# Kernel optimization log

Measured on AMD Instinct MI355X. Metric: run time of the kernel, lower is better.

## Reference

```python
import jax, jax.numpy as jnp
import numpy as np

D = 2048   # hidden_d
V = 2048   # hidden_v
L = 512    # number of points in seq
P = 64     # len(positions); decode steps = P + 1 (final special-symbol step)


def setup_inputs() -> dict:
    key = jax.random.key(0)
    ks = jax.random.split(key, 10)
    s = 0.02  # init scale for weights
    return dict(
        initial_state=jax.random.normal(ks[0], (1, D), dtype=jnp.float32),
        encoder_states=jax.random.normal(ks[1], (L + 1, D), dtype=jnp.float32),
        seq_points=jax.random.normal(ks[2], (L, 3), dtype=jnp.float32),
        positions=jax.random.randint(ks[3], (P,), 0, L),
        # LSTMCell params (torch layout: gates ordered i,f,g,o)
        W_ih=jax.random.normal(ks[4], (4 * D, 3), dtype=jnp.float32) * s,
        W_hh=jax.random.normal(ks[5], (4 * D, D), dtype=jnp.float32) * s,
        b_ih=jnp.zeros((4 * D,), dtype=jnp.float32),
        b_hh=jnp.zeros((4 * D,), dtype=jnp.float32),
        # Pointer params
        We_w=jax.random.normal(ks[6], (V, D), dtype=jnp.float32) * s,
        We_b=jnp.zeros((V,), dtype=jnp.float32),
        Wd_w=jax.random.normal(ks[7], (V, D), dtype=jnp.float32) * s,
        Wd_b=jnp.zeros((V,), dtype=jnp.float32),
        v_w=jax.random.normal(ks[8], (1, V), dtype=jnp.float32) * s,
        v_b=jnp.zeros((1,), dtype=jnp.float32),
    )


def reference(initial_state, encoder_states, seq_points, positions,
              W_ih, W_hh, b_ih, b_hh, We_w, We_b, Wd_w, Wd_b, v_w, v_b):
    """Teacher-forced pointer-network decode (positions given).

    Returns (logits [T, L+1], hidden_states [T, D], losses [T]) with
    T = len(positions) + 1 (final step targets the special symbol).
    """
    special = jnp.array([0.0, 0.0, 1.0], dtype=seq_points.dtype)
    stack_seq = jnp.concatenate([seq_points, special[None]], axis=0)  # [L+1, 3]
    Lseq = seq_points.shape[0]

    # teacher-forced inputs: step 0 = special symbol, step t = seq[positions[t-1]]
    xs = jnp.concatenate([special[None], stack_seq[positions]], axis=0)  # [T, 3]
    targets = jnp.concatenate([positions, jnp.array([Lseq])], axis=0)    # [T]

    # encoder projection is step-invariant: hoist out of the loop
    enc_proj = encoder_states @ We_w.T + We_b  # [L+1, V]

    h0 = initial_state[0]            # [D]
    c0 = jnp.zeros_like(h0)

    def step(carry, inp):
        h, c = carry
        x, tgt = inp
        gates = W_ih @ x + b_ih + W_hh @ h + b_hh  # [4D]
        i, f, g, o = jnp.split(gates, 4)
        i = jax.nn.sigmoid(i)
        f = jax.nn.sigmoid(f)
        g = jnp.tanh(g)
        o = jax.nn.sigmoid(o)
        c = f * c + i * g
        h = o * jnp.tanh(c)
        t = jnp.tanh(enc_proj + Wd_w @ h + Wd_b)   # [L+1, V]
        logits = t @ v_w[0] + v_b[0]               # [L+1]
        # CrossEntropyLoss on [1, L+1] logits with class target tgt
        loss = jax.nn.logsumexp(logits) - logits[tgt]
        return (h, c), (logits, h, loss)

    _, (logits, hs, losses) = jax.lax.scan(step, (h0, c0), (xs, targets))
    return logits, hs, losses
```

## Files before the change

kernel.cpp:

```cpp
#include <hip/hip_runtime.h>

typedef unsigned int uint32;
typedef unsigned long long u64;
typedef unsigned short u16;

#define DD    2048
#define LP1   513
#define TT    65
#define FOURD 8192
#define NWG   256
#define SLOTW 16

typedef __attribute__((ext_vector_type(8))) short short8;
typedef __attribute__((ext_vector_type(4))) float f32x4;

__device__ __forceinline__ float frcp(float x) { return __builtin_amdgcn_rcpf(x); }
__device__ __forceinline__ float sigm(float x) {
    return frcp(1.f + exp2f(-1.4426950408889634f * x));
}
__device__ __forceinline__ float tanh_fast(float x) {
    float e = exp2f(2.8853900817779268f * x);
    return fmaf(-2.f, frcp(1.f + e), 1.f);
}
__device__ __forceinline__ float bflo(uint32 w) {
    union { uint32 i; float f; } c; c.i = w << 16; return c.f;
}
__device__ __forceinline__ float bfhi(uint32 w) {
    union { uint32 i; float f; } c; c.i = w & 0xffff0000u; return c.f;
}
__device__ __forceinline__ uint32 f2bf(float f) {
    union { float f; uint32 i; } c; c.f = f;
    return (c.i + 0x7fffu + ((c.i >> 16) & 1u)) >> 16;
}
__device__ __forceinline__ uint32 pack2(float a, float b) {
    return f2bf(a) | (f2bf(b) << 16);
}

__global__ __launch_bounds__(256) void conv_bf16_kernel(
    const float* __restrict__ src, u16* __restrict__ dst)
{
    size_t i = ((size_t)blockIdx.x * 256 + threadIdx.x) * 8;
    float4 a = *(const float4*)(src + i);
    float4 b = *(const float4*)(src + i + 4);
    uint4 o;
    o.x = pack2(a.x, a.y); o.y = pack2(a.z, a.w);
    o.z = pack2(b.x, b.y); o.w = pack2(b.z, b.w);
    *(uint4*)(dst + i) = o;
}

__global__ __launch_bounds__(256) void xg_kernel(
    const float* __restrict__ W_ih, const float* __restrict__ b_ih,
    const float* __restrict__ b_hh, const float* __restrict__ seq,
    const int* __restrict__ pos, float* __restrict__ xg,
    u64* __restrict__ hX)
{
    if (blockIdx.y == 0) {
        hX[blockIdx.x * 256 + threadIdx.x] = 0ull;
    }
    int t = blockIdx.y;
    int r = blockIdx.x * 256 + threadIdx.x;
    float x0, x1, x2;
    if (t == 0) { x0 = 0.f; x1 = 0.f; x2 = 1.f; }
    else {
        int p = pos[t - 1];
        x0 = seq[p * 3 + 0]; x1 = seq[p * 3 + 1]; x2 = seq[p * 3 + 2];
    }
    float acc = b_ih[r] + b_hh[r];
    acc = fmaf(W_ih[r * 3 + 0], x0, acc);
    acc = fmaf(W_ih[r * 3 + 1], x1, acc);
    acc = fmaf(W_ih[r * 3 + 2], x2, acc);
    xg[(size_t)t * FOURD + r] = acc;
}

#define GLSTR 72
__global__ __launch_bounds__(256) void gemm_bf16_kernel(
    const u16* __restrict__ A, const u16* __restrict__ B,
    const float* __restrict__ bias, float* __restrict__ C,
    int M, int N, int K)
{
    __shared__ u16 As[64 * GLSTR];
    __shared__ u16 Bs[64 * GLSTR];
    int tid = threadIdx.x;
    int wave = tid >> 6, lane = tid & 63;
    int m0 = blockIdx.y * 64, n0 = blockIdx.x * 64;
    int wm = (wave >> 1) * 32, wn = (wave & 1) * 32;
    int srow = tid >> 2, scol = (tid & 3) * 16;

    f32x4 acc[2][2] = {};
    int fr = lane & 15, fq = (lane >> 4) * 8;
    int am = m0 + srow;
    const uint4* ap = (const uint4*)(A + (size_t)am * K + scol);
    const uint4* bp = (const uint4*)(B + (size_t)(n0 + srow) * K + scol);

    uint4 a0 = {0,0,0,0}, a1 = a0, b0, b1;
    if (am < M) { a0 = ap[0]; a1 = ap[1]; }
    b0 = bp[0]; b1 = bp[1];

    for (int k0 = 0; k0 < K; k0 += 64) {
        __syncthreads();
        {
            uint4* ad = (uint4*)(As + srow * GLSTR + scol);
            ad[0] = a0; ad[1] = a1;
            uint4* bd = (uint4*)(Bs + srow * GLSTR + scol);
            bd[0] = b0; bd[1] = b1;
        }
        __syncthreads();

        if (k0 + 64 < K) {
            int off = (k0 + 64) >> 3;
            if (am < M) { a0 = ap[off]; a1 = ap[off + 1]; }
            b0 = bp[off]; b1 = bp[off + 1];
        }

        #pragma unroll
        for (int kk = 0; kk < 64; kk += 32) {
            short8 af0 = *(const short8*)(As + (wm + fr) * GLSTR + kk + fq);
            short8 af1 = *(const short8*)(As + (wm + 16 + fr) * GLSTR + kk + fq);
            short8 bf0 = *(const short8*)(Bs + (wn + fr) * GLSTR + kk + fq);
            short8 bf1 = *(const short8*)(Bs + (wn + 16 + fr) * GLSTR + kk + fq);
            acc[0][0] = __builtin_amdgcn_mfma_f32_16x16x32_bf16(af0, bf0, acc[0][0], 0, 0, 0);
            acc[0][1] = __builtin_amdgcn_mfma_f32_16x16x32_bf16(af0, bf1, acc[0][1], 0, 0, 0);
            acc[1][0] = __builtin_amdgcn_mfma_f32_16x16x32_bf16(af1, bf0, acc[1][0], 0, 0, 0);
            acc[1][1] = __builtin_amdgcn_mfma_f32_16x16x32_bf16(af1, bf1, acc[1][1], 0, 0, 0);
        }
    }

    int cn = lane & 15, cr = (lane >> 4) * 4;
    #pragma unroll
    for (int i = 0; i < 2; i++) {
        #pragma unroll
        for (int r = 0; r < 4; r++) {
            int m = m0 + wm + i * 16 + cr + r;
            if (m < M) {
                #pragma unroll
                for (int j = 0; j < 2; j++) {
                    int n = n0 + wn + j * 16 + cn;
                    C[(size_t)m * N + n] = acc[i][j][r] + bias[n];
                }
            }
        }
    }
}

#define SMEM_FUSED (32 * 2048 * 2 + 2048 * 4 + TT * 32 * 4 + TT * 8 * 4)

__global__ __launch_bounds__(256, 1) void lstm_fused_kernel(
    const float* __restrict__ Whh, const float* __restrict__ init_h,
    const float* __restrict__ xg, u64* __restrict__ hX,
    float* __restrict__ outH, u16* __restrict__ Hb)
{
    extern __shared__ char smem[];
    u16*   Ws   = (u16*)smem;
    float* h_s  = (float*)(smem + 32 * 2048 * 2);
    float* xg_s = h_s + DD;
    float* ho_s = xg_s + TT * 32;

    int tid = threadIdx.x;
    int b = blockIdx.x;
    int wave = tid >> 6, lane = tid & 63;

    #pragma unroll 4
    for (int r = 0; r < 32; r++) {
        int g = r >> 3, j = r & 7;
        const float4* s4 =
            (const float4*)(Whh + ((size_t)(g * DD + 8 * b + j)) * DD) + tid * 2;
        float4 x = s4[0], y = s4[1];
        uint4 o;
        o.x = pack2(x.x, x.y); o.y = pack2(x.z, x.w);
        o.z = pack2(y.x, y.y); o.w = pack2(y.z, y.w);
        *(uint4*)(Ws + r * DD + tid * 8) = o;
    }
    for (int idx = tid; idx < TT * 32; idx += 256) {
        int t = idx >> 5, rr = idx & 31, g = rr >> 3, j = rr & 7;
        xg_s[idx] = xg[(size_t)t * FOURD + g * DD + 8 * b + j];
    }
    __syncthreads();

    const uint4* Wq = (const uint4*)Ws;
    int jj = lane & 1;
    int dl = 2 * wave + jj;
    float cst = 0.f;
    float4* h_s4 = (float4*)h_s;

    for (int t = 0; t < TT; t++) {
        if (t == 0) {
            const float4* hsrc = (const float4*)init_h;
            h_s4[tid] = hsrc[tid];
            h_s4[tid + 256] = hsrc[tid + 256];
        } else {
            const u64* slot = hX + ((size_t)(((t - 1) & 1) * NWG + tid)) * SLOTW;
            u64 w[8];
            for (;;) {
                bool ok = true;
                #pragma unroll
                for (int j = 0; j < 8; j++) {
                    w[j] = __hip_atomic_load(&slot[j], __ATOMIC_RELAXED,
                                             __HIP_MEMORY_SCOPE_AGENT);
                    ok &= ((uint32)(w[j] >> 32) >= (uint32)t);
                }
                if (ok) break;
                __builtin_amdgcn_s_sleep(2);
            }
            #pragma unroll
            for (int j = 0; j < 8; j++) {
                union { uint32 i; float f; } c; c.i = (uint32)w[j];
                h_s[8 * tid + j] = c.f;
            }
        }
        __syncthreads();

        float4 ha[4], hv[4];
        #pragma unroll
        for (int i = 0; i < 4; i++) {
            ha[i] = h_s4[i * 128 + lane * 2];
            hv[i] = h_s4[i * 128 + lane * 2 + 1];
        }

        float a[4][2];
        #pragma unroll
        for (int g = 0; g < 4; g++) {
            #pragma unroll
            for (int q = 0; q < 2; q++) {
                int r = g * 8 + 2 * wave + q;
                float s = 0.f;
                #pragma unroll
                for (int i = 0; i < 4; i++) {
                    uint4 ww = Wq[r * 256 + i * 64 + lane];
                    s = fmaf(bflo(ww.x), ha[i].x, s); s = fmaf(bfhi(ww.x), ha[i].y, s);
                    s = fmaf(bflo(ww.y), ha[i].z, s); s = fmaf(bfhi(ww.y), ha[i].w, s);
                    s = fmaf(bflo(ww.z), hv[i].x, s); s = fmaf(bfhi(ww.z), hv[i].y, s);
                    s = fmaf(bflo(ww.w), hv[i].z, s); s = fmaf(bfhi(ww.w), hv[i].w, s);
                }
                a[g][q] = s;
            }
        }
        #pragma unroll
        for (int off = 1; off < 64; off <<= 1) {
            #pragma unroll
            for (int g = 0; g < 4; g++) {
                a[g][0] += __shfl_xor(a[g][0], off);
                a[g][1] += __shfl_xor(a[g][1], off);
            }
        }
        float si = jj ? a[0][1] : a[0][0];
        float sf = jj ? a[1][1] : a[1][0];
        float sg = jj ? a[2][1] : a[2][0];
        float so = jj ? a[3][1] : a[3][0];
        int xb = t * 32;
        si += xg_s[xb + dl];      sf += xg_s[xb + 8 + dl];
        sg += xg_s[xb + 16 + dl]; so += xg_s[xb + 24 + dl];
        float ig = sigm(si), fg = sigm(sf), gg = tanh_fast(sg), og = sigm(so);
        cst = fmaf(fg, cst, ig * gg);
        float hh = og * tanh_fast(cst);
        if (lane < 2) {
            union { float f; uint32 i; } c; c.f = hh;
            u64 wrd = ((u64)(uint32)(t + 1) << 32) | (u64)c.i;
            __hip_atomic_store(
                &hX[((size_t)((t & 1) * NWG + b)) * SLOTW + dl], wrd,
                __ATOMIC_RELAXED, __HIP_MEMORY_SCOPE_AGENT);
            ho_s[t * 8 + dl] = hh;
        }
        __syncthreads();
    }

    for (int idx = tid; idx < TT * 8; idx += 256) {
        int t = idx >> 3, j = idx & 7;
        float hv_ = ho_s[idx];
        outH[(size_t)t * DD + 8 * b + j] = hv_;
        Hb[(size_t)t * DD + 8 * b + j] = (u16)f2bf(hv_);
    }
}

__global__ __launch_bounds__(256) void ptr_kernel(
    const float* __restrict__ enc_proj, const float* __restrict__ Dm,
    const float* __restrict__ vw, const float* __restrict__ vb,
    float* __restrict__ outL)
{
    __shared__ float vw_s[DD];
    __shared__ float Dm_s[DD];
    __shared__ float enc_s[4][DD];
    int tid = threadIdx.x;
    int l0 = blockIdx.x * 4;
    int t0 = blockIdx.y * 33;
    int nt = blockIdx.y ? 32 : 33;

    ((float4*)vw_s)[tid] = ((const float4*)vw)[tid];
    ((float4*)vw_s)[tid + 256] = ((const float4*)vw)[tid + 256];
    #pragma unroll
    for (int r = 0; r < 4; r++) {
        int l = l0 + r;
        if (l < LP1) {
            const float4* ep = (const float4*)(enc_proj + (size_t)l * DD);
            ((float4*)enc_s[r])[tid] = ep[tid];
            ((float4*)enc_s[r])[tid + 256] = ep[tid + 256];
        }
    }
    int wave = tid >> 6, lane = tid & 63;
    float vbf = vb[0];

    for (int tt = 0; tt < nt; tt++) {
        int t = t0 + tt;
        __syncthreads();
        const float4* dp = (const float4*)(Dm + (size_t)t * DD);
        ((float4*)Dm_s)[tid] = dp[tid];
        ((float4*)Dm_s)[tid + 256] = dp[tid + 256];
        __syncthreads();

        int l = l0 + wave;
        if (l < LP1) {
            const float* er = enc_s[wave];
            float acc = 0.f;
            #pragma unroll 8
            for (int i2 = 0; i2 < 32; i2++) {
                int v = lane + (i2 << 6);
                acc = fmaf(vw_s[v], tanh_fast(er[v] + Dm_s[v]), acc);
            }
            #pragma unroll
            for (int off = 1; off < 64; off <<= 1)
                acc += __shfl_xor(acc, off);
            if (lane == 0)
                outL[(size_t)t * LP1 + l] = acc + vbf;
        }
    }
}

__global__ __launch_bounds__(256) void loss_kernel(
    const float* __restrict__ LG, const int* __restrict__ pos,
    float* __restrict__ outLoss)
{
    int t = blockIdx.x, tid = threadIdx.x;
    __shared__ float red[256];
    const float* row = LG + (size_t)t * LP1;

    float m = -3.4e38f;
    for (int i = tid; i < LP1; i += 256) m = fmaxf(m, row[i]);
    red[tid] = m; __syncthreads();
    for (int s = 128; s > 0; s >>= 1) {
        if (tid < s) red[tid] = fmaxf(red[tid], red[tid + s]);
        __syncthreads();
    }
    float mx = red[0]; __syncthreads();

    float sum = 0.f;
    for (int i = tid; i < LP1; i += 256)
        sum += exp2f((row[i] - mx) * 1.4426950408889634f);
    red[tid] = sum; __syncthreads();
    for (int s = 128; s > 0; s >>= 1) {
        if (tid < s) red[tid] += red[tid + s];
        __syncthreads();
    }
    if (tid == 0) {
        int tgt = (t < TT - 1) ? pos[t] : (LP1 - 1);
        float lse = mx + 0.6931471805599453f * log2f(red[0]);
        outLoss[t] = lse - row[tgt];
    }
}

extern "C" void kernel_launch(void* const* d_in, const int* in_sizes, int n_in,
                              void* d_out, int out_size, void* d_ws, size_t ws_size,
                              hipStream_t stream) {
    const float* init_h = (const float*)d_in[0];
    const float* enc    = (const float*)d_in[1];
    const float* seq    = (const float*)d_in[2];
    const int*   pos    = (const int*)d_in[3];
    const float* W_ih   = (const float*)d_in[4];
    const float* W_hh   = (const float*)d_in[5];
    const float* b_ih   = (const float*)d_in[6];
    const float* b_hh   = (const float*)d_in[7];
    const float* We_w   = (const float*)d_in[8];
    const float* We_b   = (const float*)d_in[9];
    const float* Wd_w   = (const float*)d_in[10];
    const float* Wd_b   = (const float*)d_in[11];
    const float* v_w    = (const float*)d_in[12];
    const float* v_b    = (const float*)d_in[13];
    float* out = (float*)d_out;

    float* outL    = out;
    float* outH    = out + (size_t)TT * LP1;
    float* outLoss = outH + (size_t)TT * DD;

    float* ws = (float*)d_ws;
    float* enc_proj = ws;
    float* xg       = enc_proj + (size_t)LP1 * DD;
    float* Dm       = xg + (size_t)TT * FOURD;
    u64* hX         = (u64*)(Dm + (size_t)TT * DD);
    u16* enc_b = (u16*)(hX + 2 * NWG * SLOTW);
    u16* Web   = enc_b + (size_t)LP1 * DD;
    u16* Wdb   = Web + (size_t)DD * DD;
    u16* Hb    = Wdb + (size_t)DD * DD;

    static bool attr_done = false;
    if (!attr_done) {
        (void)hipFuncSetAttribute((const void*)lstm_fused_kernel,
                                  hipFuncAttributeMaxDynamicSharedMemorySize,
                                  SMEM_FUSED);
        attr_done = true;
    }

    conv_bf16_kernel<<<dim3(513), 256, 0, stream>>>(enc, enc_b);
    conv_bf16_kernel<<<dim3(2048), 256, 0, stream>>>(We_w, Web);
    conv_bf16_kernel<<<dim3(2048), 256, 0, stream>>>(Wd_w, Wdb);

    xg_kernel<<<dim3(32, TT), 256, 0, stream>>>(W_ih, b_ih, b_hh, seq, pos, xg,
                                                hX);

    gemm_bf16_kernel<<<dim3(32, 9), 256, 0, stream>>>(enc_b, Web, We_b, enc_proj,
                                                      LP1, DD, DD);

    {
        const float* whh = W_hh; const float* ih = init_h; const float* xgp = xg;
        u64* hx = hX; float* oh = outH; u16* hbb = Hb;
        void* kargs[] = { (void*)&whh, (void*)&ih, (void*)&xgp, (void*)&hx,
                          (void*)&oh, (void*)&hbb };
        hipError_t e = hipLaunchCooperativeKernel(
            (const void*)lstm_fused_kernel, dim3(NWG), dim3(256),
            kargs, SMEM_FUSED, stream);
        if (e != hipSuccess) {
            (void)hipGetLastError();
            lstm_fused_kernel<<<dim3(NWG), dim3(256), SMEM_FUSED, stream>>>(
                W_hh, init_h, xg, hX, outH, Hb);
        }
    }

    gemm_bf16_kernel<<<dim3(32, 2), 256, 0, stream>>>(Hb, Wdb, Wd_b, Dm,
                                                      TT, DD, DD);

    ptr_kernel<<<dim3(129, 2), 256, 0, stream>>>(enc_proj, Dm, v_w, v_b, outL);

    loss_kernel<<<TT, 256, 0, stream>>>(outL, pos, outLoss);
}
```

Measured before the change: 690.8 us.

## Register-resident LSTM weights, bf16 h exchange with per-wave LDS spin, fused conversions

The LSTM recurrence now keeps its W_hh slice in registers instead of LDS. It exchanges the hidden state as packed 16-bit bf16 plus a step tag in 32-bit words, and replaces the per-step __syncthreads with per-wave spinning on an LDS staging buffer. Dot products use the bf16 dot2 instruction when available. The separate fp32->bf16 conversion kernels are removed and the conversion is folded into the GEMM tile loads. This cuts latency on the serial 65-step critical path and saves launches, at the cost of heavy register pressure, h quantised to bf16 in the recurrence, and more complex intra-block synchronisation.

```diff
diff --git a/kernel.cpp b/kernel.cpp
--- a/kernel.cpp
+++ b/kernel.cpp
@@ -1,7 +1,6 @@
 #include <hip/hip_runtime.h>
 
 typedef unsigned int uint32;
-typedef unsigned long long u64;
 typedef unsigned short u16;
 
 #define DD    2048
@@ -9,7 +8,8 @@
 #define TT    65
 #define FOURD 8192
 #define NWG   256
-#define SLOTW 16
+#define SLOTW 32
+#define LREL  9
 
 typedef __attribute__((ext_vector_type(8))) short short8;
 typedef __attribute__((ext_vector_type(4))) float f32x4;
@@ -36,27 +36,23 @@
     return f2bf(a) | (f2bf(b) << 16);
 }
 
-__global__ __launch_bounds__(256) void conv_bf16_kernel(
-    const float* __restrict__ src, u16* __restrict__ dst)
-{
-    size_t i = ((size_t)blockIdx.x * 256 + threadIdx.x) * 8;
-    float4 a = *(const float4*)(src + i);
-    float4 b = *(const float4*)(src + i + 4);
-    uint4 o;
-    o.x = pack2(a.x, a.y); o.y = pack2(a.z, a.w);
-    o.z = pack2(b.x, b.y); o.w = pack2(b.z, b.w);
-    *(uint4*)(dst + i) = o;
-}
+#if __has_builtin(__builtin_amdgcn_fdot2_f32_bf16)
+#define HAVE_DOT2 1
+typedef __attribute__((ext_vector_type(2))) __bf16 bf16x2;
+__device__ __forceinline__ float dot2bf(uint32 a, uint32 b, float c) {
+    union { uint32 u; bf16x2 v; } x, y; x.u = a; y.u = b;
+    return __builtin_amdgcn_fdot2_f32_bf16(x.v, y.v, c, false);
+}
+#endif
 
 __global__ __launch_bounds__(256) void xg_kernel(
     const float* __restrict__ W_ih, const float* __restrict__ b_ih,
     const float* __restrict__ b_hh, const float* __restrict__ seq,
     const int* __restrict__ pos, float* __restrict__ xg,
-    u64* __restrict__ hX)
+    uint32* __restrict__ hX)
 {
-    if (blockIdx.y == 0) {
-        hX[blockIdx.x * 256 + threadIdx.x] = 0ull;
-    }
+    if (blockIdx.y < 2)
+        hX[blockIdx.y * 8192 + blockIdx.x * 256 + threadIdx.x] = 0u;
     int t = blockIdx.y;
     int r = blockIdx.x * 256 + threadIdx.x;
     float x0, x1, x2;
@@ -74,7 +70,7 @@
 
 #define GLSTR 72
 __global__ __launch_bounds__(256) void gemm_bf16_kernel(
-    const u16* __restrict__ A, const u16* __restrict__ B,
+    const float* __restrict__ A, const float* __restrict__ B,
     const float* __restrict__ bias, float* __restrict__ C,
     int M, int N, int K)
 {
@@ -89,27 +85,38 @@
     f32x4 acc[2][2] = {};
     int fr = lane & 15, fq = (lane >> 4) * 8;
     int am = m0 + srow;
-    const uint4* ap = (const uint4*)(A + (size_t)am * K + scol);
-    const uint4* bp = (const uint4*)(B + (size_t)(n0 + srow) * K + scol);
-
-    uint4 a0 = {0,0,0,0}, a1 = a0, b0, b1;
-    if (am < M) { a0 = ap[0]; a1 = ap[1]; }
-    b0 = bp[0]; b1 = bp[1];
+    const float4* ap = (const float4*)(A + (size_t)am * K + scol);
+    const float4* bp = (const float4*)(B + (size_t)(n0 + srow) * K + scol);
+
+    float4 a0 = {0,0,0,0}, a1 = a0, a2 = a0, a3 = a0, b0, b1, b2, b3;
+    if (am < M) { a0 = ap[0]; a1 = ap[1]; a2 = ap[2]; a3 = ap[3]; }
+    b0 = bp[0]; b1 = bp[1]; b2 = bp[2]; b3 = bp[3];
 
     for (int k0 = 0; k0 < K; k0 += 64) {
         __syncthreads();
         {
             uint4* ad = (uint4*)(As + srow * GLSTR + scol);
-            ad[0] = a0; ad[1] = a1;
+            uint4 o;
+            o.x = pack2(a0.x, a0.y); o.y = pack2(a0.z, a0.w);
+            o.z = pack2(a1.x, a1.y); o.w = pack2(a1.z, a1.w);
+            ad[0] = o;
+            o.x = pack2(a2.x, a2.y); o.y = pack2(a2.z, a2.w);
+            o.z = pack2(a3.x, a3.y); o.w = pack2(a3.z, a3.w);
+            ad[1] = o;
             uint4* bd = (uint4*)(Bs + srow * GLSTR + scol);
-            bd[0] = b0; bd[1] = b1;
+            o.x = pack2(b0.x, b0.y); o.y = pack2(b0.z, b0.w);
+            o.z = pack2(b1.x, b1.y); o.w = pack2(b1.z, b1.w);
+            bd[0] = o;
+            o.x = pack2(b2.x, b2.y); o.y = pack2(b2.z, b2.w);
+            o.z = pack2(b3.x, b3.y); o.w = pack2(b3.z, b3.w);
+            bd[1] = o;
         }
         __syncthreads();
 
         if (k0 + 64 < K) {
-            int off = (k0 + 64) >> 3;
-            if (am < M) { a0 = ap[off]; a1 = ap[off + 1]; }
-            b0 = bp[off]; b1 = bp[off + 1];
+            int off = (k0 + 64) >> 2;
+            if (am < M) { a0 = ap[off]; a1 = ap[off+1]; a2 = ap[off+2]; a3 = ap[off+3]; }
+            b0 = bp[off]; b1 = bp[off+1]; b2 = bp[off+2]; b3 = bp[off+3];
         }
 
         #pragma unroll
@@ -142,98 +149,141 @@
     }
 }
 
-#define SMEM_FUSED (32 * 2048 * 2 + 2048 * 4 + TT * 32 * 4 + TT * 8 * 4)
-
 __global__ __launch_bounds__(256, 1) void lstm_fused_kernel(
     const float* __restrict__ Whh, const float* __restrict__ init_h,
-    const float* __restrict__ xg, u64* __restrict__ hX,
-    float* __restrict__ outH, u16* __restrict__ Hb)
+    const float* __restrict__ xg, uint32* __restrict__ hX,
+    float* __restrict__ outH)
 {
-    extern __shared__ char smem[];
-    u16*   Ws   = (u16*)smem;
-    float* h_s  = (float*)(smem + 32 * 2048 * 2);
-    float* xg_s = h_s + DD;
-    float* ho_s = xg_s + TT * 32;
+    __shared__ float  xg_s[TT * 32];
+    __shared__ float  ho_s[TT * 8];
+    __shared__ uint32 hx_s[2 * NWG * LREL];
 
     int tid = threadIdx.x;
     int b = blockIdx.x;
     int wave = tid >> 6, lane = tid & 63;
-
-    #pragma unroll 4
-    for (int r = 0; r < 32; r++) {
-        int g = r >> 3, j = r & 7;
-        const float4* s4 =
-            (const float4*)(Whh + ((size_t)(g * DD + 8 * b + j)) * DD) + tid * 2;
-        float4 x = s4[0], y = s4[1];
-        uint4 o;
-        o.x = pack2(x.x, x.y); o.y = pack2(x.z, x.w);
-        o.z = pack2(y.x, y.y); o.w = pack2(y.z, y.w);
-        *(uint4*)(Ws + r * DD + tid * 8) = o;
-    }
+    int jj = lane & 1;
+    int dl = 2 * wave + jj;
+
+    for (int idx = tid; idx < 2 * NWG * LREL; idx += 256) hx_s[idx] = 0u;
     for (int idx = tid; idx < TT * 32; idx += 256) {
         int t = idx >> 5, rr = idx & 31, g = rr >> 3, j = rr & 7;
         xg_s[idx] = xg[(size_t)t * FOURD + g * DD + 8 * b + j];
     }
+
+    uint4 w[4][2][4];
+    #pragma unroll
+    for (int g = 0; g < 4; g++)
+        #pragma unroll
+        for (int q = 0; q < 2; q++) {
+            const float* row =
+                Whh + ((size_t)(g * DD + 8 * b + 2 * wave + q)) * DD;
+            #pragma unroll
+            for (int i = 0; i < 4; i++) {
+                const float4* p = (const float4*)(row + i * 512 + lane * 8);
+                float4 x = p[0], y = p[1];
+                uint4 o;
+                o.x = pack2(x.x, x.y); o.y = pack2(x.z, x.w);
+                o.z = pack2(y.x, y.y); o.w = pack2(y.z, y.w);
+                w[g][q][i] = o;
+            }
+        }
     __syncthreads();
 
-    const uint4* Wq = (const uint4*)Ws;
-    int jj = lane & 1;
-    int dl = 2 * wave + jj;
     float cst = 0.f;
-    float4* h_s4 = (float4*)h_s;
 
     for (int t = 0; t < TT; t++) {
+        uint32 hp[4][4];
         if (t == 0) {
-            const float4* hsrc = (const float4*)init_h;
-            h_s4[tid] = hsrc[tid];
-            h_s4[tid + 256] = hsrc[tid + 256];
+            #pragma unroll
+            for (int i = 0; i < 4; i++) {
+                const float4* p = (const float4*)(init_h + i * 512 + lane * 8);
+                float4 x = p[0], y = p[1];
+                hp[i][0] = pack2(x.x, x.y); hp[i][1] = pack2(x.z, x.w);
+                hp[i][2] = pack2(y.x, y.y); hp[i][3] = pack2(y.z, y.w);
+            }
         } else {
-            const u64* slot = hX + ((size_t)(((t - 1) & 1) * NWG + tid)) * SLOTW;
-            u64 w[8];
+            const uint32* gs =
+                hX + ((size_t)(((t - 1) & 1) * NWG + tid)) * SLOTW;
+            uint32 gv[8];
+            #pragma unroll
+            for (int j = 0; j < 8; j++)
+                gv[j] = __hip_atomic_load(gs + j, __ATOMIC_RELAXED,
+                                          __HIP_MEMORY_SCOPE_AGENT);
             for (;;) {
                 bool ok = true;
                 #pragma unroll
-                for (int j = 0; j < 8; j++) {
-                    w[j] = __hip_atomic_load(&slot[j], __ATOMIC_RELAXED,
-                                             __HIP_MEMORY_SCOPE_AGENT);
-                    ok &= ((uint32)(w[j] >> 32) >= (uint32)t);
+                for (int j = 0; j < 8; j++) ok &= ((gv[j] >> 16) >= (uint32)t);
+                if (ok) break;
+                __builtin_amdgcn_s_sleep(1);
+                #pragma unroll
+                for (int j = 0; j < 8; j++)
+                    if ((gv[j] >> 16) < (uint32)t)
+                        gv[j] = __hip_atomic_load(gs + j, __ATOMIC_RELAXED,
+                                                  __HIP_MEMORY_SCOPE_AGENT);
+            }
+            uint32* lb = hx_s + (t & 1) * (NWG * LREL);
+            #pragma unroll
+            for (int j = 0; j < 8; j++)
+                __hip_atomic_store(lb + tid * LREL + j, gv[j],
+                                   __ATOMIC_RELAXED,
+                                   __HIP_MEMORY_SCOPE_WORKGROUP);
+
+            #pragma unroll
+            for (int i = 0; i < 4; i++) {
+                const uint32* sl = lb + (i * 64 + lane) * LREL;
+                uint32 hv[8];
+                #pragma unroll
+                for (int j = 0; j < 8; j++)
+                    hv[j] = __hip_atomic_load(sl + j, __ATOMIC_RELAXED,
+                                              __HIP_MEMORY_SCOPE_WORKGROUP);
+                for (;;) {
+                    bool ok = true;
+                    #pragma unroll
+                    for (int j = 0; j < 8; j++)
+                        ok &= ((hv[j] >> 16) >= (uint32)t);
+                    if (ok) break;
+                    #pragma unroll
+                    for (int j = 0; j < 8; j++)
+                        if ((hv[j] >> 16) < (uint32)t)
+                            hv[j] = __hip_atomic_load(
+                                sl + j, __ATOMIC_RELAXED,
+                                __HIP_MEMORY_SCOPE_WORKGROUP);
                 }
-                if (ok) break;
-                __builtin_amdgcn_s_sleep(2);
-            }
-            #pragma unroll
-            for (int j = 0; j < 8; j++) {
-                union { uint32 i; float f; } c; c.i = (uint32)w[j];
-                h_s[8 * tid + j] = c.f;
-            }
-        }
-        __syncthreads();
-
-        float4 ha[4], hv[4];
-        #pragma unroll
-        for (int i = 0; i < 4; i++) {
-            ha[i] = h_s4[i * 128 + lane * 2];
-            hv[i] = h_s4[i * 128 + lane * 2 + 1];
+                hp[i][0] = (hv[0] & 0xffffu) | (hv[1] << 16);
+                hp[i][1] = (hv[2] & 0xffffu) | (hv[3] << 16);
+                hp[i][2] = (hv[4] & 0xffffu) | (hv[5] << 16);
+                hp[i][3] = (hv[6] & 0xffffu) | (hv[7] << 16);
+            }
         }
 
         float a[4][2];
         #pragma unroll
-        for (int g = 0; g < 4; g++) {
+        for (int g = 0; g < 4; g++)
             #pragma unroll
             for (int q = 0; q < 2; q++) {
-                int r = g * 8 + 2 * wave + q;
                 float s = 0.f;
                 #pragma unroll
                 for (int i = 0; i < 4; i++) {
-                    uint4 ww = Wq[r * 256 + i * 64 + lane];
-                    s = fmaf(bflo(ww.x), ha[i].x, s); s = fmaf(bfhi(ww.x), ha[i].y, s);
-                    s = fmaf(bflo(ww.y), ha[i].z, s); s = fmaf(bfhi(ww.y), ha[i].w, s);
-                    s = fmaf(bflo(ww.z), hv[i].x, s); s = fmaf(bfhi(ww.z), hv[i].y, s);
-                    s = fmaf(bflo(ww.w), hv[i].z, s); s = fmaf(bfhi(ww.w), hv[i].w, s);
+                    uint4 ww = w[g][q][i];
+#ifdef HAVE_DOT2
+                    s = dot2bf(ww.x, hp[i][0], s);
+                    s = dot2bf(ww.y, hp[i][1], s);
+                    s = dot2bf(ww.z, hp[i][2], s);
+                    s = dot2bf(ww.w, hp[i][3], s);
+#else
+                    s = fmaf(bflo(ww.x), bflo(hp[i][0]), s);
+                    s = fmaf(bfhi(ww.x), bfhi(hp[i][0]), s);
+                    s = fmaf(bflo(ww.y), bflo(hp[i][1]), s);
+                    s = fmaf(bfhi(ww.y), bfhi(hp[i][1]), s);
+                    s = fmaf(bflo(ww.z), bflo(hp[i][2]), s);
+                    s = fmaf(bfhi(ww.z), bfhi(hp[i][2]), s);
+                    s = fmaf(bflo(ww.w), bflo(hp[i][3]), s);
+                    s = fmaf(bfhi(ww.w), bfhi(hp[i][3]), s);
+#endif
                 }
                 a[g][q] = s;
             }
-        }
+
         #pragma unroll
         for (int off = 1; off < 64; off <<= 1) {
             #pragma unroll
@@ -253,21 +303,18 @@
         cst = fmaf(fg, cst, ig * gg);
         float hh = og * tanh_fast(cst);
         if (lane < 2) {
-            union { float f; uint32 i; } c; c.f = hh;
-            u64 wrd = ((u64)(uint32)(t + 1) << 32) | (u64)c.i;
+            uint32 wrd = ((uint32)(t + 1) << 16) | f2bf(hh);
             __hip_atomic_store(
                 &hX[((size_t)((t & 1) * NWG + b)) * SLOTW + dl], wrd,
                 __ATOMIC_RELAXED, __HIP_MEMORY_SCOPE_AGENT);
             ho_s[t * 8 + dl] = hh;
         }
-        __syncthreads();
-    }
-
+    }
+
+    __syncthreads();
     for (int idx = tid; idx < TT * 8; idx += 256) {
         int t = idx >> 3, j = idx & 7;
-        float hv_ = ho_s[idx];
-        outH[(size_t)t * DD + 8 * b + j] = hv_;
-        Hb[(size_t)t * DD + 8 * b + j] = (u16)f2bf(hv_);
+        outH[(size_t)t * DD + 8 * b + j] = ho_s[idx];
     }
 }
 
@@ -383,46 +430,30 @@
     float* enc_proj = ws;
     float* xg       = enc_proj + (size_t)LP1 * DD;
     float* Dm       = xg + (size_t)TT * FOURD;
-    u64* hX         = (u64*)(Dm + (size_t)TT * DD);
-    u16* enc_b = (u16*)(hX + 2 * NWG * SLOTW);
-    u16* Web   = enc_b + (size_t)LP1 * DD;
-    u16* Wdb   = Web + (size_t)DD * DD;
-    u16* Hb    = Wdb + (size_t)DD * DD;
-
-    static bool attr_done = false;
-    if (!attr_done) {
-        (void)hipFuncSetAttribute((const void*)lstm_fused_kernel,
-                                  hipFuncAttributeMaxDynamicSharedMemorySize,
-                                  SMEM_FUSED);
-        attr_done = true;
-    }
-
-    conv_bf16_kernel<<<dim3(513), 256, 0, stream>>>(enc, enc_b);
-    conv_bf16_kernel<<<dim3(2048), 256, 0, stream>>>(We_w, Web);
-    conv_bf16_kernel<<<dim3(2048), 256, 0, stream>>>(Wd_w, Wdb);
+    uint32* hX      = (uint32*)(Dm + (size_t)TT * DD);
 
     xg_kernel<<<dim3(32, TT), 256, 0, stream>>>(W_ih, b_ih, b_hh, seq, pos, xg,
                                                 hX);
 
-    gemm_bf16_kernel<<<dim3(32, 9), 256, 0, stream>>>(enc_b, Web, We_b, enc_proj,
+    gemm_bf16_kernel<<<dim3(32, 9), 256, 0, stream>>>(enc, We_w, We_b, enc_proj,
                                                       LP1, DD, DD);
 
     {
         const float* whh = W_hh; const float* ih = init_h; const float* xgp = xg;
-        u64* hx = hX; float* oh = outH; u16* hbb = Hb;
+        uint32* hx = hX; float* oh = outH;
         void* kargs[] = { (void*)&whh, (void*)&ih, (void*)&xgp, (void*)&hx,
-                          (void*)&oh, (void*)&hbb };
+                          (void*)&oh };
         hipError_t e = hipLaunchCooperativeKernel(
             (const void*)lstm_fused_kernel, dim3(NWG), dim3(256),
-            kargs, SMEM_FUSED, stream);
+            kargs, 0, stream);
         if (e != hipSuccess) {
             (void)hipGetLastError();
-            lstm_fused_kernel<<<dim3(NWG), dim3(256), SMEM_FUSED, stream>>>(
-                W_hh, init_h, xg, hX, outH, Hb);
-        }
-    }
-
-    gemm_bf16_kernel<<<dim3(32, 2), 256, 0, stream>>>(Hb, Wdb, Wd_b, Dm,
+            lstm_fused_kernel<<<dim3(NWG), dim3(256), 0, stream>>>(
+                W_hh, init_h, xg, hX, outH);
+        }
+    }
+
+    gemm_bf16_kernel<<<dim3(32, 2), 256, 0, stream>>>(outH, Wd_w, Wd_b, Dm,
                                                       TT, DD, DD);
 
     ptr_kernel<<<dim3(129, 2), 256, 0, stream>>>(enc_proj, Dm, v_w, v_b, outL);
```

Measured after the change: 902.5 us. +30.7%, slower.

## Exchange LSTM hidden state as packed bf16 flags and use bf16 dot2

Applied to the files above, without the earlier changes.

The cross-workgroup hidden-state exchange now uses 32-bit words that pack a 16-bit step tag with a bf16 hidden value, instead of 64-bit words holding a 32-bit tag and an fp32 value. Polling reloads only the words that are not yet ready and sleeps for a shorter time. Each thread pulls the packed bf16 h from a padded shared buffer, and the recurrent matvec uses the bf16 dot2 instruction, which cuts the unpack work and drops one barrier per step. The cost is that h enters the matvec rounded to bf16, which may add error that compounds over the 65 recurrent steps.

```diff
diff --git a/kernel.cpp b/kernel.cpp
--- a/kernel.cpp
+++ b/kernel.cpp
@@ -1,7 +1,6 @@
 #include <hip/hip_runtime.h>
 
 typedef unsigned int uint32;
-typedef unsigned long long u64;
 typedef unsigned short u16;
 
 #define DD    2048
@@ -9,7 +8,8 @@
 #define TT    65
 #define FOURD 8192
 #define NWG   256
-#define SLOTW 16
+#define SLOTW 32
+#define PSTR  5
 
 typedef __attribute__((ext_vector_type(8))) short short8;
 typedef __attribute__((ext_vector_type(4))) float f32x4;
@@ -35,6 +35,15 @@
 __device__ __forceinline__ uint32 pack2(float a, float b) {
     return f2bf(a) | (f2bf(b) << 16);
 }
+
+#if __has_builtin(__builtin_amdgcn_fdot2_f32_bf16)
+#define HAVE_DOT2 1
+typedef __attribute__((ext_vector_type(2))) __bf16 bf16x2;
+__device__ __forceinline__ float dot2bf(uint32 a, uint32 b, float c) {
+    union { uint32 u; bf16x2 v; } x, y; x.u = a; y.u = b;
+    return __builtin_amdgcn_fdot2_f32_bf16(x.v, y.v, c, false);
+}
+#endif
 
 __global__ __launch_bounds__(256) void conv_bf16_kernel(
     const float* __restrict__ src, u16* __restrict__ dst)
@@ -52,11 +61,10 @@
     const float* __restrict__ W_ih, const float* __restrict__ b_ih,
     const float* __restrict__ b_hh, const float* __restrict__ seq,
     const int* __restrict__ pos, float* __restrict__ xg,
-    u64* __restrict__ hX)
-{
-    if (blockIdx.y == 0) {
-        hX[blockIdx.x * 256 + threadIdx.x] = 0ull;
-    }
+    uint32* __restrict__ hX)
+{
+    if (blockIdx.y < 2)
+        hX[blockIdx.y * 8192 + blockIdx.x * 256 + threadIdx.x] = 0u;
     int t = blockIdx.y;
     int r = blockIdx.x * 256 + threadIdx.x;
     float x0, x1, x2;
@@ -142,22 +150,24 @@
     }
 }
 
-#define SMEM_FUSED (32 * 2048 * 2 + 2048 * 4 + TT * 32 * 4 + TT * 8 * 4)
+#define SMEM_FUSED (32 * 2048 * 2 + TT * 32 * 4 + TT * 8 * 4 + NWG * PSTR * 4)
 
 __global__ __launch_bounds__(256, 1) void lstm_fused_kernel(
     const float* __restrict__ Whh, const float* __restrict__ init_h,
-    const float* __restrict__ xg, u64* __restrict__ hX,
+    const float* __restrict__ xg, uint32* __restrict__ hX,
     float* __restrict__ outH, u16* __restrict__ Hb)
 {
     extern __shared__ char smem[];
-    u16*   Ws   = (u16*)smem;
-    float* h_s  = (float*)(smem + 32 * 2048 * 2);
-    float* xg_s = h_s + DD;
-    float* ho_s = xg_s + TT * 32;
+    u16*    Ws   = (u16*)smem;
+    float*  xg_s = (float*)(smem + 32 * 2048 * 2);
+    float*  ho_s = xg_s + TT * 32;
+    uint32* hp_s = (uint32*)(ho_s + TT * 8);
 
     int tid = threadIdx.x;
     int b = blockIdx.x;
     int wave = tid >> 6, lane = tid & 63;
+    int jj = lane & 1;
+    int dl = 2 * wave + jj;
 
     #pragma unroll 4
     for (int r = 0; r < 32; r++) {
@@ -177,48 +187,55 @@
     __syncthreads();
 
     const uint4* Wq = (const uint4*)Ws;
-    int jj = lane & 1;
-    int dl = 2 * wave + jj;
     float cst = 0.f;
-    float4* h_s4 = (float4*)h_s;
 
     for (int t = 0; t < TT; t++) {
+        uint32 hp[4][4];
         if (t == 0) {
-            const float4* hsrc = (const float4*)init_h;
-            h_s4[tid] = hsrc[tid];
-            h_s4[tid + 256] = hsrc[tid + 256];
+            #pragma unroll
+            for (int i = 0; i < 4; i++) {
+                const float4* p = (const float4*)(init_h + i * 512 + lane * 8);
+                float4 x = p[0], y = p[1];
+                hp[i][0] = pack2(x.x, x.y); hp[i][1] = pack2(x.z, x.w);
+                hp[i][2] = pack2(y.x, y.y); hp[i][3] = pack2(y.z, y.w);
+            }
         } else {
-            const u64* slot = hX + ((size_t)(((t - 1) & 1) * NWG + tid)) * SLOTW;
-            u64 w[8];
+            const uint32* gs =
+                hX + ((size_t)(((t - 1) & 1) * NWG + tid)) * SLOTW;
+            uint32 gv[8];
+            #pragma unroll
+            for (int j = 0; j < 8; j++)
+                gv[j] = __hip_atomic_load(gs + j, __ATOMIC_RELAXED,
+                                          __HIP_MEMORY_SCOPE_AGENT);
             for (;;) {
                 bool ok = true;
                 #pragma unroll
-                for (int j = 0; j < 8; j++) {
-                    w[j] = __hip_atomic_load(&slot[j], __ATOMIC_RELAXED,
-                                             __HIP_MEMORY_SCOPE_AGENT);
-                    ok &= ((uint32)(w[j] >> 32) >= (uint32)t);
-                }
+                for (int j = 0; j < 8; j++) ok &= ((gv[j] >> 16) >= (uint32)t);
                 if (ok) break;
-                __builtin_amdgcn_s_sleep(2);
-            }
-            #pragma unroll
-            for (int j = 0; j < 8; j++) {
-                union { uint32 i; float f; } c; c.i = (uint32)w[j];
-                h_s[8 * tid + j] = c.f;
-            }
-        }
-        __syncthreads();
-
-        float4 ha[4], hv[4];
-        #pragma unroll
-        for (int i = 0; i < 4; i++) {
-            ha[i] = h_s4[i * 128 + lane * 2];
-            hv[i] = h_s4[i * 128 + lane * 2 + 1];
+                __builtin_amdgcn_s_sleep(1);
+                #pragma unroll
+                for (int j = 0; j < 8; j++)
+                    if ((gv[j] >> 16) < (uint32)t)
+                        gv[j] = __hip_atomic_load(gs + j, __ATOMIC_RELAXED,
+                                                  __HIP_MEMORY_SCOPE_AGENT);
+            }
+            hp_s[tid * PSTR + 0] = (gv[0] & 0xffffu) | (gv[1] << 16);
+            hp_s[tid * PSTR + 1] = (gv[2] & 0xffffu) | (gv[3] << 16);
+            hp_s[tid * PSTR + 2] = (gv[4] & 0xffffu) | (gv[5] << 16);
+            hp_s[tid * PSTR + 3] = (gv[6] & 0xffffu) | (gv[7] << 16);
+            __syncthreads();
+
+            #pragma unroll
+            for (int i = 0; i < 4; i++) {
+                const uint32* sl = hp_s + (i * 64 + lane) * PSTR;
+                hp[i][0] = sl[0]; hp[i][1] = sl[1];
+                hp[i][2] = sl[2]; hp[i][3] = sl[3];
+            }
         }
 
         float a[4][2];
         #pragma unroll
-        for (int g = 0; g < 4; g++) {
+        for (int g = 0; g < 4; g++)
             #pragma unroll
             for (int q = 0; q < 2; q++) {
                 int r = g * 8 + 2 * wave + q;
@@ -226,14 +243,25 @@
                 #pragma unroll
                 for (int i = 0; i < 4; i++) {
                     uint4 ww = Wq[r * 256 + i * 64 + lane];
-                    s = fmaf(bflo(ww.x), ha[i].x, s); s = fmaf(bfhi(ww.x), ha[i].y, s);
-                    s = fmaf(bflo(ww.y), ha[i].z, s); s = fmaf(bfhi(ww.y), ha[i].w, s);
-                    s = fmaf(bflo(ww.z), hv[i].x, s); s = fmaf(bfhi(ww.z), hv[i].y, s);
-                    s = fmaf(bflo(ww.w), hv[i].z, s); s = fmaf(bfhi(ww.w), hv[i].w, s);
+#ifdef HAVE_DOT2
+                    s = dot2bf(ww.x, hp[i][0], s);
+                    s = dot2bf(ww.y, hp[i][1], s);
+                    s = dot2bf(ww.z, hp[i][2], s);
+                    s = dot2bf(ww.w, hp[i][3], s);
+#else
+                    s = fmaf(bflo(ww.x), bflo(hp[i][0]), s);
+                    s = fmaf(bfhi(ww.x), bfhi(hp[i][0]), s);
+                    s = fmaf(bflo(ww.y), bflo(hp[i][1]), s);
+                    s = fmaf(bfhi(ww.y), bfhi(hp[i][1]), s);
+                    s = fmaf(bflo(ww.z), bflo(hp[i][2]), s);
+                    s = fmaf(bfhi(ww.z), bfhi(hp[i][2]), s);
+                    s = fmaf(bflo(ww.w), bflo(hp[i][3]), s);
+                    s = fmaf(bfhi(ww.w), bfhi(hp[i][3]), s);
+#endif
                 }
                 a[g][q] = s;
             }
-        }
+
         #pragma unroll
         for (int off = 1; off < 64; off <<= 1) {
             #pragma unroll
@@ -253,16 +281,16 @@
         cst = fmaf(fg, cst, ig * gg);
         float hh = og * tanh_fast(cst);
         if (lane < 2) {
-            union { float f; uint32 i; } c; c.f = hh;
-            u64 wrd = ((u64)(uint32)(t + 1) << 32) | (u64)c.i;
+            uint32 wrd = ((uint32)(t + 1) << 16) | f2bf(hh);
             __hip_atomic_store(
                 &hX[((size_t)((t & 1) * NWG + b)) * SLOTW + dl], wrd,
                 __ATOMIC_RELAXED, __HIP_MEMORY_SCOPE_AGENT);
             ho_s[t * 8 + dl] = hh;
         }
-        __syncthreads();
-    }
-
+        if (t > 0) __syncthreads();
+    }
+
+    __syncthreads();
     for (int idx = tid; idx < TT * 8; idx += 256) {
         int t = idx >> 3, j = idx & 7;
         float hv_ = ho_s[idx];
@@ -383,7 +411,7 @@
     float* enc_proj = ws;
     float* xg       = enc_proj + (size_t)LP1 * DD;
     float* Dm       = xg + (size_t)TT * FOURD;
-    u64* hX         = (u64*)(Dm + (size_t)TT * DD);
+    uint32* hX      = (uint32*)(Dm + (size_t)TT * DD);
     u16* enc_b = (u16*)(hX + 2 * NWG * SLOTW);
     u16* Web   = enc_b + (size_t)LP1 * DD;
     u16* Wdb   = Web + (size_t)DD * DD;
@@ -409,7 +437,7 @@
 
     {
         const float* whh = W_hh; const float* ih = init_h; const float* xgp = xg;
-        u64* hx = hX; float* oh = outH; u16* hbb = Hb;
+        uint32* hx = hX; float* oh = outH; u16* hbb = Hb;
         void* kargs[] = { (void*)&whh, (void*)&ih, (void*)&xgp, (void*)&hx,
                           (void*)&oh, (void*)&hbb };
         hipError_t e = hipLaunchCooperativeKernel(
```

After: 633.0 us. 1.09x faster.
